# Kernel optimization log

Measured on AMD Instinct MI355X. Metric: run time of the kernel, lower is better.

The kernel has to match this reference:

```python
import jax, jax.numpy as jnp
import numpy as np


def euler_xyz_to_matrix(angles):
    # pytorch3d euler_angles_to_matrix(angles, 'XYZ') = R_X(a0) @ R_Y(a1) @ R_Z(a2)
    ax, ay, az = angles[..., 0], angles[..., 1], angles[..., 2]
    cx, sx = jnp.cos(ax), jnp.sin(ax)
    cy, sy = jnp.cos(ay), jnp.sin(ay)
    cz, sz = jnp.cos(az), jnp.sin(az)
    one = jnp.ones_like(ax)
    zero = jnp.zeros_like(ax)
    Rx = jnp.stack([one, zero, zero, zero, cx, -sx, zero, sx, cx], axis=-1).reshape(*ax.shape, 3, 3)
    Ry = jnp.stack([cy, zero, sy, zero, one, zero, -sy, zero, cy], axis=-1).reshape(*ax.shape, 3, 3)
    Rz = jnp.stack([cz, -sz, zero, sz, cz, zero, zero, zero, one], axis=-1).reshape(*ax.shape, 3, 3)
    return Rx @ Ry @ Rz


def chamfer_bidir(x, y):
    # x, y: [R, I, N, 3]. Squared-distance chamfer, mean point reduction, per (R,I) batch.
    x2 = jnp.sum(x * x, axis=-1)  # [R,I,N]
    y2 = jnp.sum(y * y, axis=-1)  # [R,I,N]
    # d2[r,i,n,m] = |x_n - y_m|^2
    d2 = x2[..., :, None] + y2[..., None, :] - 2.0 * jnp.einsum('rind,rimd->rinm', x, y)
    cham_x = jnp.mean(jnp.min(d2, axis=-1), axis=-1)  # x -> nearest y
    cham_y = jnp.mean(jnp.min(d2, axis=-2), axis=-1)  # y -> nearest x
    return cham_x + cham_y  # [R, I]


def setup_inputs() -> dict:
    key = jax.random.key(0)
    k1, k2, k3, k4 = jax.random.split(key, 4)
    R, I, N = 4, 16, 2048
    source_points = jax.random.normal(k1, (R, I, N, 3), dtype=jnp.float32)
    target_points = jax.random.normal(k2, (I, N, 3), dtype=jnp.float32)
    rotation = 0.1 * jax.random.normal(k3, (R, I, 3), dtype=jnp.float32)
    translation = 0.1 * jax.random.normal(k4, (R, I, 3), dtype=jnp.float32)
    scale = jnp.ones((R, I), dtype=jnp.float32)
    return {
        'source_points': source_points,
        'target_points': target_points,
        'rotation': rotation,
        'translation': translation,
        'scale': scale,
    }


def reference(source_points, target_points, rotation, translation, scale):
    R, I, N, _ = source_points.shape
    rot = euler_xyz_to_matrix(rotation)  # [R,I,3,3]
    # Transform per original: 4x4 matrix with rows [:3,:] scaled by `scale`,
    # so p' = scale * (rot @ p + translation).
    transformed = scale[..., None, None] * (
        jnp.einsum('rind,rikd->rink', source_points, rot) + translation[..., None, :]
    )  # [R,I,N,3]
    # target_points [I,N,3] broadcast to [R,I,N,3] (original repeats along R)
    target = jnp.broadcast_to(target_points[None], transformed.shape)
    # original calls chamfer_distance(target, transformed): x=target, y=transformed
    return chamfer_bidir(target, transformed)  # [R, I]
```

## Files before the change

### kernel.cpp

```cpp
#include <hip/hip_runtime.h>
#include <math.h>

#define RDIM 4
#define IDIM 16
#define NPAIR 64
#define NPTS 2048
#define THREADS 256
#define ROWSB 256
#define RBLK (NPTS / ROWSB)
#define TILES (NPTS / 32)
#define SCRS 64
#define PSPLIT 4
#define ONEBF 0x3F80u

typedef __attribute__((ext_vector_type(8))) short bf16x8;
typedef __attribute__((ext_vector_type(16))) float f32x16;
typedef __attribute__((ext_vector_type(4))) float f32x4;

__device__ __forceinline__ float min3f(float a, float b, float c) {
    return fminf(a, fminf(b, c));
}

__device__ __forceinline__ unsigned int f2bf(float f) {
    union { float f; unsigned int u; } v; v.f = f;
    return (v.u + 0x7FFFu + ((v.u >> 16) & 1u)) >> 16;
}
__device__ __forceinline__ float bf2f(unsigned int h) {
    union { unsigned int u; float f; } v; v.u = h << 16; return v.f;
}

__device__ __forceinline__ void make_rot(const float* __restrict__ rotv, int pair,
                                         float& r00, float& r01, float& r02,
                                         float& r10, float& r11, float& r12,
                                         float& r20, float& r21, float& r22) {
    const float ax = rotv[pair * 3 + 0];
    const float ay = rotv[pair * 3 + 1];
    const float az = rotv[pair * 3 + 2];
    float sx, cx, sy, cy, sz, cz;
    sincosf(ax, &sx, &cx);
    sincosf(ay, &sy, &cy);
    sincosf(az, &sz, &cz);
    r00 = cy * cz;                r01 = -cy * sz;               r02 = sy;
    r10 = cx * sz + sx * sy * cz; r11 = cx * cz - sx * sy * sz; r12 = -sx * cy;
    r20 = sx * sz - cx * sy * cz; r21 = sx * cz + cx * sy * sz; r22 = cx * cy;
}

__device__ __forceinline__ uint4 brec(float v0, float v1, float v2) {
    const float b0 = -2.0f * v0, b1 = -2.0f * v1, b2 = -2.0f * v2;
    const unsigned int h0 = f2bf(b0), h1 = f2bf(b1), h2 = f2bf(b2);
    const unsigned int l0 = f2bf(b0 - bf2f(h0));
    const unsigned int l1 = f2bf(b1 - bf2f(h1));
    const unsigned int l2 = f2bf(b2 - bf2f(h2));
    const float n2 = v0 * v0 + v1 * v1 + v2 * v2;
    const unsigned int nh = f2bf(n2), nl = f2bf(n2 - bf2f(nh));
    return make_uint4(h0 | (h1 << 16), h2 | (l0 << 16), l1 | (l2 << 16), nh | (nl << 16));
}
__device__ __forceinline__ void arec(float q0, float q1, float q2, uint4& a0, uint4& a1) {
    const unsigned int h0 = f2bf(q0), h1 = f2bf(q1), h2 = f2bf(q2);
    const unsigned int l0 = f2bf(q0 - bf2f(h0));
    const unsigned int l1 = f2bf(q1 - bf2f(h1));
    const unsigned int l2 = f2bf(q2 - bf2f(h2));
    a0 = make_uint4(h0 | (h1 << 16), h2 | (l0 << 16), l1 | (l2 << 16), ONEBF);
    a1 = make_uint4(l0 | (l1 << 16), l2 | (h0 << 16), h1 | (h2 << 16), ONEBF << 16);
}

__global__ __launch_bounds__(THREADS)
void prep(const float* __restrict__ src, const float* __restrict__ tgt,
          const float* __restrict__ rotv, const float* __restrict__ trav,
          const float* __restrict__ scal,
          uint4* __restrict__ Yb, uint4* __restrict__ Ya,
          uint4* __restrict__ Xb, uint4* __restrict__ Xa)
{
    const int b   = blockIdx.x;
    const int seg = blockIdx.y;
    const int tid = threadIdx.x;
    const int m0  = seg * (NPTS / PSPLIT);
    if (b < NPAIR) {
        const int pair = b;
        float r00, r01, r02, r10, r11, r12, r20, r21, r22;
        make_rot(rotv, pair, r00, r01, r02, r10, r11, r12, r20, r21, r22);
        const float t0 = trav[pair * 3 + 0];
        const float t1 = trav[pair * 3 + 1];
        const float t2 = trav[pair * 3 + 2];
        const float s  = scal[pair];
        const float* __restrict__ srcp = src + (size_t)pair * NPTS * 3;
#pragma unroll
        for (int u = 0; u < NPTS / THREADS / PSPLIT; ++u) {
            const int m = m0 + u * THREADS + tid;
            const float p0 = srcp[m * 3 + 0];
            const float p1 = srcp[m * 3 + 1];
            const float p2 = srcp[m * 3 + 2];
            const float y0 = s * fmaf(r00, p0, fmaf(r01, p1, fmaf(r02, p2, t0)));
            const float y1 = s * fmaf(r10, p0, fmaf(r11, p1, fmaf(r12, p2, t1)));
            const float y2 = s * fmaf(r20, p0, fmaf(r21, p1, fmaf(r22, p2, t2)));
            Yb[(size_t)pair * NPTS + m] = brec(y0, y1, y2);
            uint4 a0, a1;
            arec(y0, y1, y2, a0, a1);
            Ya[((size_t)pair * NPTS + m) * 2 + 0] = a0;
            Ya[((size_t)pair * NPTS + m) * 2 + 1] = a1;
        }
    } else {
        const int i = b - NPAIR;
        const float* __restrict__ tgtp = tgt + (size_t)i * NPTS * 3;
#pragma unroll
        for (int u = 0; u < NPTS / THREADS / PSPLIT; ++u) {
            const int m = m0 + u * THREADS + tid;
            const float x0 = tgtp[m * 3 + 0];
            const float x1 = tgtp[m * 3 + 1];
            const float x2 = tgtp[m * 3 + 2];
            Xb[(size_t)i * NPTS + m] = brec(x0, x1, x2);
            uint4 a0, a1;
            arec(x0, x1, x2, a0, a1);
            Xa[((size_t)i * NPTS + m) * 2 + 0] = a0;
            Xa[((size_t)i * NPTS + m) * 2 + 1] = a1;
        }
    }
}

__global__ __launch_bounds__(THREADS, 3)
void chamfer_main(const uint4* __restrict__ Yb, const uint4* __restrict__ Ya,
                  const uint4* __restrict__ Xb, const uint4* __restrict__ Xa,
                  float* __restrict__ out, const float czero)
{
    __shared__ alignas(16) unsigned char smem[32768 + 8192];
    __shared__ float wsum[4];
    unsigned short* sB = (unsigned short*)smem;
    float* scratch = (float*)smem;
    unsigned short* sA = (unsigned short*)(smem + 32768);

    const int pair  = blockIdx.x;
    const int rb    = blockIdx.y;
    const int passB = blockIdx.z;
    const int i     = pair & (IDIM - 1);
    const int tid   = threadIdx.x;
    const int lane  = tid & 63;
    const int w     = tid >> 6;
    const int c31   = lane & 31;
    const int h     = lane >> 5;

    const uint4* __restrict__ gB = (passB == 0) ? (Yb + (size_t)pair * NPTS)
                                                : (Xb + (size_t)i * NPTS);
    const uint4* __restrict__ gA = (passB == 0)
        ? (Xa + ((size_t)i * NPTS + rb * ROWSB) * 2)
        : (Ya + ((size_t)pair * NPTS + rb * ROWSB) * 2);

#pragma unroll
    for (int j = 0; j < 8; ++j)
        ((uint4*)sB)[j * THREADS + tid] = gB[j * THREADS + tid];
    ((uint4*)sA)[tid] = gA[tid];
    ((uint4*)sA)[THREADS + tid] = gA[THREADS + tid];
    __syncthreads();

    bf16x8 af[2];
    af[0] = *(const bf16x8*)&sA[(w * 64 + c31) * 16 + h * 8];
    af[1] = *(const bf16x8*)&sA[(w * 64 + 32 + c31) * 16 + h * 8];

    float mn[2][16];
#pragma unroll
    for (int rt = 0; rt < 2; ++rt)
#pragma unroll
        for (int j = 0; j < 16; ++j) mn[rt][j] = 3.4e38f;

    f32x16 zero16;
#pragma unroll
    for (int j = 0; j < 16; ++j) zero16[j] = czero;

#pragma unroll 2
    for (int t = 0; t < TILES; t += 2) {
        const bf16x8 bfA = *(const bf16x8*)&sB[((t + 0) * 32 + c31) * 8];
        const bf16x8 bfB = *(const bf16x8*)&sB[((t + 1) * 32 + c31) * 8];
        const f32x16 a0 = __builtin_amdgcn_mfma_f32_32x32x16_bf16(af[0], bfA, zero16, 0, 0, 0);
        const f32x16 b0 = __builtin_amdgcn_mfma_f32_32x32x16_bf16(af[0], bfB, zero16, 0, 0, 0);
#pragma unroll
        for (int j = 0; j < 16; ++j)
            mn[0][j] = min3f(mn[0][j], a0[j], b0[j]);
        const f32x16 a1 = __builtin_amdgcn_mfma_f32_32x32x16_bf16(af[1], bfA, zero16, 0, 0, 0);
        const f32x16 b1 = __builtin_amdgcn_mfma_f32_32x32x16_bf16(af[1], bfB, zero16, 0, 0, 0);
#pragma unroll
        for (int j = 0; j < 16; ++j)
            mn[1][j] = min3f(mn[1][j], a1[j], b1[j]);
    }
    __syncthreads();

#pragma unroll
    for (int rt = 0; rt < 2; ++rt)
#pragma unroll
        for (int g2 = 0; g2 < 4; ++g2) {
            const int rowb = (rt * 32 + 8 * g2 + 4 * h) ^ ((c31 & 7) << 2);
            f32x4 v4;
            v4[0] = mn[rt][g2 * 4 + 0];
            v4[1] = mn[rt][g2 * 4 + 1];
            v4[2] = mn[rt][g2 * 4 + 2];
            v4[3] = mn[rt][g2 * 4 + 3];
            *(f32x4*)&scratch[(w * 32 + c31) * SCRS + rowb] = v4;
        }
    __syncthreads();

    float m = fminf(scratch[(w * 32 + 0) * SCRS + lane],
                    scratch[(w * 32 + 31) * SCRS + (lane ^ ((31 & 7) << 2))]);
#pragma unroll
    for (int c = 1; c < 31; c += 2)
        m = min3f(m, scratch[(w * 32 + c) * SCRS + (lane ^ ((c & 7) << 2))],
                     scratch[(w * 32 + c + 1) * SCRS + (lane ^ (((c + 1) & 7) << 2))]);

    const unsigned short* ar = &sA[tid * 16];
    const float q0 = bf2f(ar[0]) + bf2f(ar[3]);
    const float q1 = bf2f(ar[1]) + bf2f(ar[4]);
    const float q2 = bf2f(ar[2]) + bf2f(ar[5]);
    float v = m + q0 * q0 + q1 * q1 + q2 * q2;

#pragma unroll
    for (int off = 32; off > 0; off >>= 1)
        v += __shfl_down(v, off, 64);
    if (lane == 0) wsum[w] = v;
    __syncthreads();
    if (tid == 0) {
        const float tot = wsum[0] + wsum[1] + wsum[2] + wsum[3];
        atomicAdd(&out[pair], tot * (1.0f / NPTS));
    }
}

extern "C" void kernel_launch(void* const* d_in, const int* in_sizes, int n_in,
                              void* d_out, int out_size, void* d_ws, size_t ws_size,
                              hipStream_t stream) {
    const float* src  = (const float*)d_in[0];
    const float* tgt  = (const float*)d_in[1];
    const float* rotv = (const float*)d_in[2];
    const float* trav = (const float*)d_in[3];
    const float* scal = (const float*)d_in[4];
    float* out = (float*)d_out;

    char* ws = (char*)d_ws;
    uint4* Yb = (uint4*)ws;
    uint4* Ya = (uint4*)(ws + (size_t)NPAIR * NPTS * 16);
    uint4* Xb = (uint4*)(ws + (size_t)NPAIR * NPTS * 48);
    uint4* Xa = (uint4*)(ws + (size_t)NPAIR * NPTS * 48 + (size_t)IDIM * NPTS * 16);

    hipMemsetAsync(out, 0, NPAIR * sizeof(float), stream);

    dim3 pgrid(NPAIR + IDIM, PSPLIT);
    prep<<<pgrid, THREADS, 0, stream>>>(src, tgt, rotv, trav, scal, Yb, Ya, Xb, Xa);

    dim3 grid(NPAIR, RBLK, 2);
    chamfer_main<<<grid, THREADS, 0, stream>>>(Yb, Ya, Xb, Xa, out, 0.0f);
}
```

Measured before the change: 100.2 us.

## Switch chamfer min-distance MFMA from 32x32x16 to 16x16x32 tiles

```diff
diff --git a/kernel.cpp b/kernel.cpp
--- a/kernel.cpp
+++ b/kernel.cpp
@@ -8,13 +8,11 @@
 #define THREADS 256
 #define ROWSB 256
 #define RBLK (NPTS / ROWSB)
-#define TILES (NPTS / 32)
-#define SCRS 64
+#define T16 (NPTS / 16)
 #define PSPLIT 4
 #define ONEBF 0x3F80u
 
 typedef __attribute__((ext_vector_type(8))) short bf16x8;
-typedef __attribute__((ext_vector_type(16))) float f32x16;
 typedef __attribute__((ext_vector_type(4))) float f32x4;
 
 __device__ __forceinline__ float min3f(float a, float b, float c) {
@@ -117,16 +115,15 @@
     }
 }
 
-__global__ __launch_bounds__(THREADS, 3)
+__global__ __launch_bounds__(THREADS, 4)
 void chamfer_main(const uint4* __restrict__ Yb, const uint4* __restrict__ Ya,
                   const uint4* __restrict__ Xb, const uint4* __restrict__ Xa,
                   float* __restrict__ out, const float czero)
 {
-    __shared__ alignas(16) unsigned char smem[32768 + 8192];
+    __shared__ alignas(16) unsigned char smem[32768];
+    __shared__ float rowmin[ROWSB];
     __shared__ float wsum[4];
     unsigned short* sB = (unsigned short*)smem;
-    float* scratch = (float*)smem;
-    unsigned short* sA = (unsigned short*)(smem + 32768);
 
     const int pair  = blockIdx.x;
     const int rb    = blockIdx.y;
@@ -135,75 +132,78 @@
     const int tid   = threadIdx.x;
     const int lane  = tid & 63;
     const int w     = tid >> 6;
-    const int c31   = lane & 31;
-    const int h     = lane >> 5;
+    const int c15   = lane & 15;
+    const int hi    = lane >> 4;
 
     const uint4* __restrict__ gB = (passB == 0) ? (Yb + (size_t)pair * NPTS)
                                                 : (Xb + (size_t)i * NPTS);
     const uint4* __restrict__ gA = (passB == 0)
         ? (Xa + ((size_t)i * NPTS + rb * ROWSB) * 2)
         : (Ya + ((size_t)pair * NPTS + rb * ROWSB) * 2);
+    const char* gAb = (const char*)gA;
 
 #pragma unroll
     for (int j = 0; j < 8; ++j)
         ((uint4*)sB)[j * THREADS + tid] = gB[j * THREADS + tid];
-    ((uint4*)sA)[tid] = gA[tid];
-    ((uint4*)sA)[THREADS + tid] = gA[THREADS + tid];
+
+    const bf16x8 zero8 = {0, 0, 0, 0, 0, 0, 0, 0};
+    bf16x8 af[4];
+#pragma unroll
+    for (int rt = 0; rt < 4; ++rt) {
+        const int row = w * 64 + rt * 16 + c15;
+        af[rt] = (hi < 2) ? *(const bf16x8*)(gAb + row * 32 + hi * 16) : zero8;
+    }
+
+    f32x4 zero4;
+    zero4[0] = czero; zero4[1] = czero; zero4[2] = czero; zero4[3] = czero;
+
+    float mn[4][4];
+#pragma unroll
+    for (int rt = 0; rt < 4; ++rt)
+#pragma unroll
+        for (int j = 0; j < 4; ++j) mn[rt][j] = 3.4e38f;
+
     __syncthreads();
 
-    bf16x8 af[2];
-    af[0] = *(const bf16x8*)&sA[(w * 64 + c31) * 16 + h * 8];
-    af[1] = *(const bf16x8*)&sA[(w * 64 + 32 + c31) * 16 + h * 8];
-
-    float mn[2][16];
-#pragma unroll
-    for (int rt = 0; rt < 2; ++rt)
-#pragma unroll
-        for (int j = 0; j < 16; ++j) mn[rt][j] = 3.4e38f;
-
-    f32x16 zero16;
-#pragma unroll
-    for (int j = 0; j < 16; ++j) zero16[j] = czero;
-
 #pragma unroll 2
-    for (int t = 0; t < TILES; t += 2) {
-        const bf16x8 bfA = *(const bf16x8*)&sB[((t + 0) * 32 + c31) * 8];
-        const bf16x8 bfB = *(const bf16x8*)&sB[((t + 1) * 32 + c31) * 8];
-        const f32x16 a0 = __builtin_amdgcn_mfma_f32_32x32x16_bf16(af[0], bfA, zero16, 0, 0, 0);
-        const f32x16 b0 = __builtin_amdgcn_mfma_f32_32x32x16_bf16(af[0], bfB, zero16, 0, 0, 0);
-#pragma unroll
-        for (int j = 0; j < 16; ++j)
-            mn[0][j] = min3f(mn[0][j], a0[j], b0[j]);
-        const f32x16 a1 = __builtin_amdgcn_mfma_f32_32x32x16_bf16(af[1], bfA, zero16, 0, 0, 0);
-        const f32x16 b1 = __builtin_amdgcn_mfma_f32_32x32x16_bf16(af[1], bfB, zero16, 0, 0, 0);
-#pragma unroll
-        for (int j = 0; j < 16; ++j)
-            mn[1][j] = min3f(mn[1][j], a1[j], b1[j]);
+    for (int t = 0; t < T16; t += 2) {
+        const bf16x8 bf0 = *(const bf16x8*)&sB[((t + 0) * 16 + c15) * 8];
+        const bf16x8 bf1 = *(const bf16x8*)&sB[((t + 1) * 16 + c15) * 8];
+#pragma unroll
+        for (int rt = 0; rt < 4; ++rt) {
+            const f32x4 d0 = __builtin_amdgcn_mfma_f32_16x16x32_bf16(af[rt], bf0, zero4, 0, 0, 0);
+            const f32x4 d1 = __builtin_amdgcn_mfma_f32_16x16x32_bf16(af[rt], bf1, zero4, 0, 0, 0);
+#pragma unroll
+            for (int j = 0; j < 4; ++j)
+                mn[rt][j] = min3f(mn[rt][j], d0[j], d1[j]);
+        }
+    }
+
+#pragma unroll
+    for (int rt = 0; rt < 4; ++rt)
+#pragma unroll
+        for (int j = 0; j < 4; ++j) {
+            float v = mn[rt][j];
+            v = fminf(v, __shfl_xor(v, 1, 64));
+            v = fminf(v, __shfl_xor(v, 2, 64));
+            v = fminf(v, __shfl_xor(v, 4, 64));
+            v = fminf(v, __shfl_xor(v, 8, 64));
+            mn[rt][j] = v;
+        }
+
+    if (c15 == 0) {
+#pragma unroll
+        for (int rt = 0; rt < 4; ++rt) {
+            f32x4 v4;
+            v4[0] = mn[rt][0]; v4[1] = mn[rt][1];
+            v4[2] = mn[rt][2]; v4[3] = mn[rt][3];
+            *(f32x4*)&rowmin[w * 64 + rt * 16 + hi * 4] = v4;
+        }
     }
     __syncthreads();
 
-#pragma unroll
-    for (int rt = 0; rt < 2; ++rt)
-#pragma unroll
-        for (int g2 = 0; g2 < 4; ++g2) {
-            const int rowb = (rt * 32 + 8 * g2 + 4 * h) ^ ((c31 & 7) << 2);
-            f32x4 v4;
-            v4[0] = mn[rt][g2 * 4 + 0];
-            v4[1] = mn[rt][g2 * 4 + 1];
-            v4[2] = mn[rt][g2 * 4 + 2];
-            v4[3] = mn[rt][g2 * 4 + 3];
-            *(f32x4*)&scratch[(w * 32 + c31) * SCRS + rowb] = v4;
-        }
-    __syncthreads();
-
-    float m = fminf(scratch[(w * 32 + 0) * SCRS + lane],
-                    scratch[(w * 32 + 31) * SCRS + (lane ^ ((31 & 7) << 2))]);
-#pragma unroll
-    for (int c = 1; c < 31; c += 2)
-        m = min3f(m, scratch[(w * 32 + c) * SCRS + (lane ^ ((c & 7) << 2))],
-                     scratch[(w * 32 + c + 1) * SCRS + (lane ^ (((c + 1) & 7) << 2))]);
-
-    const unsigned short* ar = &sA[tid * 16];
+    const float m = rowmin[tid];
+    const unsigned short* ar = (const unsigned short*)(gAb + tid * 32);
     const float q0 = bf2f(ar[0]) + bf2f(ar[3]);
     const float q1 = bf2f(ar[1]) + bf2f(ar[4]);
     const float q2 = bf2f(ar[2]) + bf2f(ar[5]);
```

Measured after the change: 105.5 us. 1.05x slower.
